# Optimization experiments

Measured on AMD Instinct MI355X. Metric: run time of the kernel, lower is better.

Reference implementation:

```python
import jax, jax.numpy as jnp
import numpy as np

T, B, N = 16, 32, 4096
NUM_TYPES = 20
F = NUM_TYPES + 5  # 4 geo feats + one-hot type + valid flag
H = 8              # poly_hidden_layers
HID = 128          # hidden_layers


def _w(k, i, o):
    return jax.random.normal(k, (i, o), jnp.float32) / np.sqrt(i)


def setup_inputs() -> dict:
    key = jax.random.key(0)
    ks = jax.random.split(key, 8)
    points = jax.random.normal(ks[0], (T, B, N, F), jnp.float32)
    return {
        "points": points,
        "W1": _w(ks[1], F, H), "b1": jnp.zeros((H,), jnp.float32),
        "W2": _w(ks[2], H, H), "b2": jnp.zeros((H,), jnp.float32),
        "W3": _w(ks[3], H, H), "b3": jnp.zeros((H,), jnp.float32),
        "W4": _w(ks[4], 2 * H, H), "b4": jnp.zeros((H,), jnp.float32),
        "W5": _w(ks[5], H, H), "b5": jnp.zeros((H,), jnp.float32),
        "W6": _w(ks[6], H, H), "b6": jnp.zeros((H,), jnp.float32),
        "Wout": _w(ks[7], NUM_TYPES * H, HID), "bout": jnp.zeros((HID,), jnp.float32),
    }


def reference(points, W1, b1, W2, b2, W3, b3, W4, b4, W5, b5, W6, b6, Wout, bout):
    t, b, n, f = points.shape
    nt = f - 5
    x = points.reshape(t * b * n, f)
    valid = (x[:, -1:] != 0)                      # (TBN,1) nonzero == True, as jnp.where on floats
    types = jnp.argmax(x[:, 4:-1], axis=1)        # (TBN,) polyline type per point

    h = jax.nn.relu(x @ W1 + b1)
    h = jax.nn.relu(h @ W2 + b2)
    h = jax.nn.relu(h @ W3 + b3)
    h = jnp.where(valid, h, 0.0)                  # zero-out invalid points

    # segment id = (t,b) slot * num_types + type; pooling is per (t,b,type)
    tb = jnp.arange(t * b * n) // n
    seg = tb * nt + types
    num_seg = t * b * nt
    # original masks non-matching points to 0 then takes max over N; since h >= 0
    # (relu + zero masking), that equals max(segment_max, 0); empty types -> 0.
    pooled = jnp.maximum(jax.ops.segment_max(h, seg, num_segments=num_seg), 0.0)

    h = jnp.concatenate([h, pooled[seg]], axis=-1)  # (TBN, 2H)
    h = jax.nn.relu(h @ W4 + b4)
    h = jax.nn.relu(h @ W5 + b5)
    h = jax.nn.relu(h @ W6 + b6)
    h = jnp.where(valid, h, 0.0)

    pooled2 = jnp.maximum(jax.ops.segment_max(h, seg, num_segments=num_seg), 0.0)
    out = pooled2.reshape(t, b, nt * h.shape[-1])   # types concatenated along feature dim
    return jax.nn.relu(out @ Wout + bout)           # (T, B, hidden_layers)
```

## Files before the change

kernel.cpp:

```cpp
#include <hip/hip_runtime.h>

#define T_ 16
#define B_ 32
#define N_ 4096
#define NT 20
#define F_ 25
#define H_ 8
#define HID_ 128
#define PSTR 9
#define SEGF_ (NT*H_)
#define BT 512
#define NSUB (N_/BT)
#define CF (BT*F_)
#define WSL 1600

typedef __attribute__((address_space(1))) const void GV;
typedef __attribute__((address_space(3))) void LV;

__device__ __forceinline__ void g2l16(const float* g, float* l) {
  __builtin_amdgcn_global_load_lds((GV*)g, (LV*)l, 16, 0, 0);
}
__device__ __forceinline__ void g2l4(const float* g, float* l) {
  __builtin_amdgcn_global_load_lds((GV*)g, (LV*)l, 4, 0, 0);
}

__device__ __forceinline__ float bf2f(unsigned s) { return __uint_as_float(s << 16); }

__device__ __forceinline__ unsigned cvtpk_bf16(float lo, float hi) {
  unsigned r;
  asm("v_cvt_pk_bf16_f32 %0, %1, %2" : "=v"(r) : "v"(lo), "v"(hi));
  return r;
}

__device__ __forceinline__ void pkfma(float2& acc, float a,
                                      const float* __restrict__ wp) {
  const float2 w = *(const float2*)wp;
  float2 a2; a2.x = a; a2.y = a;
  asm("v_pk_fma_f32 %0, %1, %2, %0" : "+v"(acc) : "v"(a2), "s"(w));
}

template<int NI>
__device__ __forceinline__ void layerP(const float* in, const float* __restrict__ W,
                                       const float* __restrict__ b, float* out) {
  float2 acc[4];
#pragma unroll
  for (int jp = 0; jp < 4; jp++) acc[jp] = *(const float2*)&b[jp*2];
#pragma unroll
  for (int f = 0; f < NI; f++) {
#pragma unroll
    for (int jp = 0; jp < 4; jp++) pkfma(acc[jp], in[f], &W[f*H_ + jp*2]);
  }
#pragma unroll
  for (int jp = 0; jp < 4; jp++) {
    out[jp*2]   = fmaxf(acc[jp].x, 0.0f);
    out[jp*2+1] = fmaxf(acc[jp].y, 0.0f);
  }
}

__device__ __forceinline__ void layerPc(const float* in, const float* __restrict__ W,
                                        const float* ctbp, float* out) {
  float2 acc[4];
#pragma unroll
  for (int jp = 0; jp < 4; jp++) acc[jp] = *(const float2*)&ctbp[jp*2];
#pragma unroll
  for (int f = 0; f < H_; f++) {
#pragma unroll
    for (int jp = 0; jp < 4; jp++) pkfma(acc[jp], in[f], &W[f*H_ + jp*2]);
  }
#pragma unroll
  for (int jp = 0; jp < 4; jp++) {
    out[jp*2]   = fmaxf(acc[jp].x, 0.0f);
    out[jp*2+1] = fmaxf(acc[jp].y, 0.0f);
  }
}

extern "C" __global__ __launch_bounds__(BT, 4)
void kFused(const float* __restrict__ pts,
            const float* __restrict__ W1, const float* __restrict__ b1,
            const float* __restrict__ W2, const float* __restrict__ b2,
            const float* __restrict__ W3, const float* __restrict__ b3,
            const float* __restrict__ W4, const float* __restrict__ b4,
            const float* __restrict__ W5, const float* __restrict__ b5,
            const float* __restrict__ W6, const float* __restrict__ b6,
            const float* __restrict__ Wout, const float* __restrict__ bout,
            float* __restrict__ out)
{
  __shared__ float xs[8*WSL];
  __shared__ int lp1[NT*PSTR];
  __shared__ int lp2[NT*PSTR];
  __shared__ float ctb[NT*H_];
  const int tid  = threadIdx.x;
  const int wid  = tid >> 6;
  const int lane = tid & 63;
  const int tb = blockIdx.x;
  if (tid < NT*PSTR) { lp1[tid] = 0; lp2[tid] = 0; }
  __syncthreads();

  const float* base = pts + (size_t)tb * (N_*F_);
  float* lw = xs + wid*WSL;

#define ISSUE(S)                                                         \
  {                                                                      \
    const float* gw = base + (S)*CF + wid*WSL;                           \
    _Pragma("unroll")                                                    \
    for (int k = 0; k < 6; k++)                                          \
      g2l16(gw + k*256 + lane*4, lw + k*256 + lane*4);                   \
    g2l4(gw + 1536 + lane, lw + 1536 + lane);                            \
  }

  uint4 h3p[NSUB];
  int   tyv[NSUB];

  ISSUE(0)

#define PH1(S)                                                           \
  {                                                                      \
    asm volatile("s_waitcnt vmcnt(0)" ::: "memory");                     \
    __builtin_amdgcn_sched_barrier(0);                                   \
    float xv[F_];                                                        \
    _Pragma("unroll")                                                    \
    for (int f = 0; f < F_; f++) xv[f] = lw[lane*F_ + f];                \
    asm volatile("s_waitcnt lgkmcnt(0)" ::: "memory");                   \
    __builtin_amdgcn_sched_barrier(0);                                   \
    if ((S) < NSUB-1) ISSUE((S)+1)                                       \
    int ty = 0; float best = xv[4];                                      \
    _Pragma("unroll")                                                    \
    for (int k = 1; k < NT; k++)                                         \
      if (xv[4+k] > best) { best = xv[4+k]; ty = k; }                    \
    const bool valid = (xv[F_-1] != 0.0f);                               \
    float t1[H_], t2[H_];                                                \
    layerP<F_>(xv, W1, b1, t1);                                          \
    layerP<H_>(t1, W2, b2, t2);                                          \
    layerP<H_>(t2, W3, b3, t1);                                          \
    if (!valid) {                                                        \
      _Pragma("unroll")                                                  \
      for (int j = 0; j < H_; j++) t1[j] = 0.0f;                         \
    }                                                                    \
    h3p[S].x = cvtpk_bf16(t1[0], t1[1]);                                 \
    h3p[S].y = cvtpk_bf16(t1[2], t1[3]);                                 \
    h3p[S].z = cvtpk_bf16(t1[4], t1[5]);                                 \
    h3p[S].w = cvtpk_bf16(t1[6], t1[7]);                                 \
    tyv[S] = valid ? ty : -1;                                            \
    if (valid) {                                                         \
      _Pragma("unroll")                                                  \
      for (int j = 0; j < H_; j++)                                       \
        atomicMax(&lp1[ty*PSTR + j], __float_as_int(t1[j]));             \
    }                                                                    \
  }

  PH1(0) PH1(1) PH1(2) PH1(3) PH1(4) PH1(5) PH1(6) PH1(7)

  __syncthreads();

  if (tid < NT*H_) {
    const int cty = tid >> 3, cj = tid & 7;
    float a = b4[cj];
#pragma unroll
    for (int k = 0; k < H_; k++)
      a = fmaf(__int_as_float(lp1[cty*PSTR + k]), W4[(H_+k)*H_ + cj], a);
    ctb[tid] = a;
  }
  __syncthreads();

#define PH2(S)                                                           \
  {                                                                      \
    const int ty = tyv[S];                                               \
    if (ty >= 0) {                                                       \
      float x8[H_];                                                      \
      x8[0] = bf2f(h3p[S].x & 0xffffu); x8[1] = bf2f(h3p[S].x >> 16);    \
      x8[2] = bf2f(h3p[S].y & 0xffffu); x8[3] = bf2f(h3p[S].y >> 16);    \
      x8[4] = bf2f(h3p[S].z & 0xffffu); x8[5] = bf2f(h3p[S].z >> 16);    \
      x8[6] = bf2f(h3p[S].w & 0xffffu); x8[7] = bf2f(h3p[S].w >> 16);    \
      float t1[H_], t2[H_];                                              \
      layerPc(x8, W4, &ctb[ty*H_], t1);                                  \
      layerP<H_>(t1, W5, b5, t2);                                        \
      layerP<H_>(t2, W6, b6, t1);                                        \
      _Pragma("unroll")                                                  \
      for (int j = 0; j < H_; j++)                                       \
        atomicMax(&lp2[ty*PSTR + j], __float_as_int(t1[j]));             \
    }                                                                    \
  }

  PH2(0) PH2(1) PH2(2) PH2(3) PH2(4) PH2(5) PH2(6) PH2(7)

  __syncthreads();

  if (tid < HID_) {
    float a = bout[tid];
#pragma unroll 4
    for (int k = 0; k < SEGF_; k++) {
      const float v = __int_as_float(lp2[(k >> 3)*PSTR + (k & 7)]);
      a = fmaf(v, Wout[k*HID_ + tid], a);
    }
    out[tb*HID_ + tid] = fmaxf(a, 0.0f);
  }
#undef ISSUE
#undef PH1
#undef PH2
}

extern "C" void kernel_launch(void* const* d_in, const int* in_sizes, int n_in,
                              void* d_out, int out_size, void* d_ws, size_t ws_size,
                              hipStream_t stream) {
  const float* pts  = (const float*)d_in[0];
  const float* W1   = (const float*)d_in[1];  const float* b1 = (const float*)d_in[2];
  const float* W2   = (const float*)d_in[3];  const float* b2 = (const float*)d_in[4];
  const float* W3   = (const float*)d_in[5];  const float* b3 = (const float*)d_in[6];
  const float* W4   = (const float*)d_in[7];  const float* b4 = (const float*)d_in[8];
  const float* W5   = (const float*)d_in[9];  const float* b5 = (const float*)d_in[10];
  const float* W6   = (const float*)d_in[11]; const float* b6 = (const float*)d_in[12];
  const float* Wout = (const float*)d_in[13]; const float* bout = (const float*)d_in[14];
  float* out = (float*)d_out;

  kFused<<<T_*B_, BT, 0, stream>>>(pts, W1, b1, W2, b2, W3, b3,
                                   W4, b4, W5, b5, W6, b6, Wout, bout, out);
}
```

Measured before the change: 62.51 us.

## Replace LDS-staged point loads with direct register double-buffered loads, 1024 threads

Drops the global-to-LDS async staging and instead loads each point's 25 features straight into registers as 16-byte vectors. The next chunk is prefetched into a second register set (double buffering). Block size doubles to 1024 threads, so each thread handles 4 points instead of 8. This removes the LDS round trip and waitcnt barriers, at the cost of uncoalesced per-thread strided global loads and higher register pressure under the launch bounds.

```diff
diff --git a/kernel.cpp b/kernel.cpp
--- a/kernel.cpp
+++ b/kernel.cpp
@@ -9,20 +9,10 @@
 #define HID_ 128
 #define PSTR 9
 #define SEGF_ (NT*H_)
-#define BT 512
-#define NSUB (N_/BT)
-#define CF (BT*F_)
-#define WSL 1600
-
-typedef __attribute__((address_space(1))) const void GV;
-typedef __attribute__((address_space(3))) void LV;
-
-__device__ __forceinline__ void g2l16(const float* g, float* l) {
-  __builtin_amdgcn_global_load_lds((GV*)g, (LV*)l, 16, 0, 0);
-}
-__device__ __forceinline__ void g2l4(const float* g, float* l) {
-  __builtin_amdgcn_global_load_lds((GV*)g, (LV*)l, 4, 0, 0);
-}
+#define BT 1024
+#define NCH 4
+
+typedef float f32x4 __attribute__((ext_vector_type(4), aligned(4)));
 
 __device__ __forceinline__ float bf2f(unsigned s) { return __uint_as_float(s << 16); }
 
@@ -72,6 +62,31 @@
     out[jp*2]   = fmaxf(acc[jp].x, 0.0f);
     out[jp*2+1] = fmaxf(acc[jp].y, 0.0f);
   }
+}
+
+struct PtRegs { f32x4 q0, q1, q2, q3, q4, q5; float qt; };
+
+__device__ __forceinline__ void loadPt(PtRegs& d, const float* __restrict__ px) {
+  const f32x4* p4 = (const f32x4*)px;
+  d.q0 = p4[0]; d.q1 = p4[1]; d.q2 = p4[2];
+  d.q3 = p4[3]; d.q4 = p4[4]; d.q5 = p4[5];
+  d.qt = px[24];
+}
+
+__device__ __forceinline__ void toArr(const PtRegs& p, float* xv) {
+#pragma unroll
+  for (int k = 0; k < 4; k++) xv[k]      = p.q0[k];
+#pragma unroll
+  for (int k = 0; k < 4; k++) xv[4+k]    = p.q1[k];
+#pragma unroll
+  for (int k = 0; k < 4; k++) xv[8+k]    = p.q2[k];
+#pragma unroll
+  for (int k = 0; k < 4; k++) xv[12+k]   = p.q3[k];
+#pragma unroll
+  for (int k = 0; k < 4; k++) xv[16+k]   = p.q4[k];
+#pragma unroll
+  for (int k = 0; k < 4; k++) xv[20+k]   = p.q5[k];
+  xv[24] = p.qt;
 }
 
 extern "C" __global__ __launch_bounds__(BT, 4)
@@ -85,44 +100,28 @@
             const float* __restrict__ Wout, const float* __restrict__ bout,
             float* __restrict__ out)
 {
-  __shared__ float xs[8*WSL];
   __shared__ int lp1[NT*PSTR];
   __shared__ int lp2[NT*PSTR];
   __shared__ float ctb[NT*H_];
-  const int tid  = threadIdx.x;
-  const int wid  = tid >> 6;
-  const int lane = tid & 63;
+  const int tid = threadIdx.x;
   const int tb = blockIdx.x;
   if (tid < NT*PSTR) { lp1[tid] = 0; lp2[tid] = 0; }
   __syncthreads();
 
   const float* base = pts + (size_t)tb * (N_*F_);
-  float* lw = xs + wid*WSL;
-
-#define ISSUE(S)                                                         \
+
+  uint4 h3p[NCH];
+  int   tyv[NCH];
+
+  PtRegs pA, pB;
+  loadPt(pA, base + (size_t)tid * F_);
+
+#define PH1(S, CUR, NXT)                                                 \
   {                                                                      \
-    const float* gw = base + (S)*CF + wid*WSL;                           \
-    _Pragma("unroll")                                                    \
-    for (int k = 0; k < 6; k++)                                          \
-      g2l16(gw + k*256 + lane*4, lw + k*256 + lane*4);                   \
-    g2l4(gw + 1536 + lane, lw + 1536 + lane);                            \
-  }
-
-  uint4 h3p[NSUB];
-  int   tyv[NSUB];
-
-  ISSUE(0)
-
-#define PH1(S)                                                           \
-  {                                                                      \
-    asm volatile("s_waitcnt vmcnt(0)" ::: "memory");                     \
-    __builtin_amdgcn_sched_barrier(0);                                   \
+    if ((S) < NCH-1)                                                     \
+      loadPt(NXT, base + (size_t)(((S)+1)*BT + tid) * F_);               \
     float xv[F_];                                                        \
-    _Pragma("unroll")                                                    \
-    for (int f = 0; f < F_; f++) xv[f] = lw[lane*F_ + f];                \
-    asm volatile("s_waitcnt lgkmcnt(0)" ::: "memory");                   \
-    __builtin_amdgcn_sched_barrier(0);                                   \
-    if ((S) < NSUB-1) ISSUE((S)+1)                                       \
+    toArr(CUR, xv);                                                      \
     int ty = 0; float best = xv[4];                                      \
     _Pragma("unroll")                                                    \
     for (int k = 1; k < NT; k++)                                         \
@@ -148,7 +147,7 @@
     }                                                                    \
   }
 
-  PH1(0) PH1(1) PH1(2) PH1(3) PH1(4) PH1(5) PH1(6) PH1(7)
+  PH1(0, pA, pB) PH1(1, pB, pA) PH1(2, pA, pB) PH1(3, pB, pA)
 
   __syncthreads();
 
@@ -181,7 +180,7 @@
     }                                                                    \
   }
 
-  PH2(0) PH2(1) PH2(2) PH2(3) PH2(4) PH2(5) PH2(6) PH2(7)
+  PH2(0) PH2(1) PH2(2) PH2(3)
 
   __syncthreads();
 
@@ -194,7 +193,6 @@
     }
     out[tb*HID_ + tid] = fmaxf(a, 0.0f);
   }
-#undef ISSUE
 #undef PH1
 #undef PH2
 }
```

After: 71.78 us. 14.8% more time.
